# Performance work log

Hardware: AMD Instinct MI355X
Metric: run time of the kernel (lower is better)

Reference implementation:

```python
import jax, jax.numpy as jnp
import numpy as np

NUM_HEADS = 12
EPS = 1e-6


def setup_inputs() -> dict:
    key = jax.random.key(0)
    k1, k2, k3, k4, k5 = jax.random.split(key, 5)
    B, N, C = 8, 4096, 768
    scale = 1.0 / np.sqrt(C)
    return {
        "x": jax.random.normal(k1, (B, N, C), dtype=jnp.float32),
        "W_qkv": jax.random.normal(k2, (C, 3 * C), dtype=jnp.float32) * scale,
        "b_qkv": jax.random.normal(k3, (3 * C,), dtype=jnp.float32) * 0.02,
        "W_proj": jax.random.normal(k4, (C, C), dtype=jnp.float32) * scale,
        "b_proj": jax.random.normal(k5, (C,), dtype=jnp.float32) * 0.02,
    }


def reference(x, W_qkv, b_qkv, W_proj, b_proj):
    B, N, C = x.shape
    H = NUM_HEADS
    D = C // H
    # qkv projection -> (3, B, H, N, D)
    qkv = (x @ W_qkv + b_qkv).reshape(B, N, 3, H, D).transpose(2, 0, 3, 1, 4)
    q, k, v = qkv[0], qkv[1], qkv[2]
    q = jax.nn.sigmoid(q)
    k = jax.nn.sigmoid(k)
    ksum = k.sum(axis=2)  # [B,H,D]
    qsum = q.sum(axis=2)  # [B,H,D]
    # incoming/outgoing flow normalizers, [B,H,N]
    sink_incoming = 1.0 / (jnp.einsum('bhnd,bhd->bhn', q + EPS, ksum + EPS) + EPS)
    source_outgoing = 1.0 / (jnp.einsum('bhnd,bhd->bhn', k + EPS, qsum + EPS) + EPS)
    conserved_sink = jnp.einsum(
        'bhnd,bhd->bhn', q + EPS, (k * source_outgoing[..., None]).sum(axis=2) + EPS) + EPS
    conserved_source = jnp.einsum(
        'bhnd,bhd->bhn', k + EPS, (q * sink_incoming[..., None]).sum(axis=2) + EPS) + EPS
    conserved_source = jnp.clip(conserved_source, -1.0, 1.0)
    sink_allocation = jax.nn.sigmoid(conserved_sink * (float(N) / float(N)))
    source_competition = jax.nn.softmax(conserved_source, axis=-1) * float(N)
    # linear attention: kv = k^T @ (v * competition), [B,H,D,D]
    kv = jnp.einsum('bhnd,bhne->bhde', k, v * source_competition[..., None])
    x_update = jnp.einsum('bhnd,bhde->bhne', q, kv)
    x_update = x_update * sink_incoming[..., None] * sink_allocation[..., None]
    out = x_update.transpose(0, 2, 1, 3).reshape(B, N, C)
    out = out @ W_proj + b_proj
    return jax.nn.sigmoid(2.0 * out)
```

## Files before the change

### kernel.cpp

```cpp
#include <hip/hip_runtime.h>
#include <stdint.h>

#define EPSF 1e-6f

typedef unsigned short u16;
typedef __attribute__((ext_vector_type(8))) short short8;
typedef __attribute__((ext_vector_type(4))) float f32x4;

__device__ __forceinline__ float us2f(u16 u) {
  union { float f; unsigned int i; } c; c.i = ((unsigned int)u) << 16; return c.f;
}
__device__ __forceinline__ u16 f2bfu(float f) {
  union { float f; unsigned int i; } c; c.f = f;
  unsigned int i = c.i;
  return (u16)((i + 0x7FFFu + ((i >> 16) & 1u)) >> 16);
}
__device__ __forceinline__ float sigm(float x) { return 1.f / (1.f + __expf(-x)); }

typedef __attribute__((address_space(3))) unsigned int lds_u32;
typedef const __attribute__((address_space(1))) unsigned int glb_u32;
__device__ __forceinline__ void gl_lds16(const u16* g, u16* l) {
  __builtin_amdgcn_global_load_lds((glb_u32*)g, (lds_u32*)l, 16, 0, 0);
}

__global__ void k_cvt_x(const float* __restrict__ in, u16* __restrict__ out) {
  const int i = blockIdx.x * 256 + threadIdx.x;
  float4 v = ((const float4*)in)[i];
  ushort4 o;
  o.x = f2bfu(v.x); o.y = f2bfu(v.y); o.z = f2bfu(v.z); o.w = f2bfu(v.w);
  ((ushort4*)out)[i] = o;
}

__global__ void k_transpose(const float* __restrict__ in, u16* __restrict__ out, int R, int C) {
  __shared__ float tile[32][33];
  const int tx = threadIdx.x & 31, ty = threadIdx.x >> 5;
  const int c0 = blockIdx.x << 5, r0 = blockIdx.y << 5;
  for (int i = ty; i < 32; i += 8) tile[i][tx] = in[(size_t)(r0 + i) * C + c0 + tx];
  __syncthreads();
  for (int i = ty; i < 32; i += 8) out[(size_t)(c0 + i) * R + r0 + tx] = f2bfu(tile[tx][i]);
}

template <int MODE>
__global__ __launch_bounds__(512, 1) void k_gemm(
    const u16* __restrict__ A, const u16* __restrict__ BT,
    const float* __restrict__ bias,
    u16* __restrict__ qkvo, float* __restrict__ qsum, float* __restrict__ ksum,
    float* __restrict__ outf)
{
  __shared__ __align__(16) u16 smem[65536];
  const int tid = threadIdx.x;
  const int lane = tid & 63;
  const int wid = tid >> 6;
  const int wm = wid >> 2, wn = wid & 3;
  const int nx = gridDim.x;
  int lid = blockIdx.y * nx + blockIdx.x;
  const int q8 = (nx * gridDim.y) >> 3;
  lid = (lid & 7) * q8 + (lid >> 3);
  const int m0 = (lid / nx) << 8;
  const int n0 = (lid % nx) << 8;

  const int rowL0 = tid >> 3;
  const int gc = (tid & 7) ^ (rowL0 & 7);
  const u16* gA = A  + (size_t)(m0 + rowL0) * 768 + (gc << 3);
  const u16* gB = BT + (size_t)(n0 + rowL0) * 768 + (gc << 3);

  const int r16 = lane & 15;
  const int sgrp = lane >> 4;
  const int xk = r16 & 7;
  const int coff0 = ((sgrp) ^ xk) << 3;
  const int coff1 = ((4 + sgrp) ^ xk) << 3;
  const int bbase = ((wn & 1) << 6) + r16;

  f32x4 acc[8][4];
#pragma unroll
  for (int i = 0; i < 8; ++i)
#pragma unroll
    for (int j = 0; j < 4; ++j) acc[i][j] = (f32x4){0.f, 0.f, 0.f, 0.f};

#define STAGEU(tt, y)                                                         \
  do {                                                                        \
    u16* dst = &smem[(((((tt) & 1) << 2) | (y)) << 13) + (tid << 3)];         \
    const u16* s = (((y) < 2) ? gA + (size_t)(y) * 98304                      \
                              : gB + (size_t)((y) - 2) * 98304) + (tt) * 64;  \
    gl_lds16(s, dst);                                                         \
    gl_lds16(s + 49152, dst + 4096);                                          \
  } while (0)

#define RDA(mi, co) (*(const short8*)(pa + ((((mi) << 4) + r16) << 6) + (co)))
#define RDB(nj, co) (*(const short8*)(pb + ((bbase + ((nj) << 4)) << 6) + (co)))

#define MFMA16(P, A00, A01, A10, A11)                                                               \
  do {                                                                                              \
    acc[2*(P)  ][0] = __builtin_amdgcn_mfma_f32_16x16x32_bf16(A00, bf[0][0], acc[2*(P)  ][0],0,0,0);\
    acc[2*(P)  ][1] = __builtin_amdgcn_mfma_f32_16x16x32_bf16(A00, bf[1][0], acc[2*(P)  ][1],0,0,0);\
    acc[2*(P)  ][2] = __builtin_amdgcn_mfma_f32_16x16x32_bf16(A00, bf[2][0], acc[2*(P)  ][2],0,0,0);\
    acc[2*(P)  ][3] = __builtin_amdgcn_mfma_f32_16x16x32_bf16(A00, bf[3][0], acc[2*(P)  ][3],0,0,0);\
    acc[2*(P)+1][0] = __builtin_amdgcn_mfma_f32_16x16x32_bf16(A10, bf[0][0], acc[2*(P)+1][0],0,0,0);\
    acc[2*(P)+1][1] = __builtin_amdgcn_mfma_f32_16x16x32_bf16(A10, bf[1][0], acc[2*(P)+1][1],0,0,0);\
    acc[2*(P)+1][2] = __builtin_amdgcn_mfma_f32_16x16x32_bf16(A10, bf[2][0], acc[2*(P)+1][2],0,0,0);\
    acc[2*(P)+1][3] = __builtin_amdgcn_mfma_f32_16x16x32_bf16(A10, bf[3][0], acc[2*(P)+1][3],0,0,0);\
    acc[2*(P)  ][0] = __builtin_amdgcn_mfma_f32_16x16x32_bf16(A01, bf[0][1], acc[2*(P)  ][0],0,0,0);\
    acc[2*(P)  ][1] = __builtin_amdgcn_mfma_f32_16x16x32_bf16(A01, bf[1][1], acc[2*(P)  ][1],0,0,0);\
    acc[2*(P)  ][2] = __builtin_amdgcn_mfma_f32_16x16x32_bf16(A01, bf[2][1], acc[2*(P)  ][2],0,0,0);\
    acc[2*(P)  ][3] = __builtin_amdgcn_mfma_f32_16x16x32_bf16(A01, bf[3][1], acc[2*(P)  ][3],0,0,0);\
    acc[2*(P)+1][0] = __builtin_amdgcn_mfma_f32_16x16x32_bf16(A11, bf[0][1], acc[2*(P)+1][0],0,0,0);\
    acc[2*(P)+1][1] = __builtin_amdgcn_mfma_f32_16x16x32_bf16(A11, bf[1][1], acc[2*(P)+1][1],0,0,0);\
    acc[2*(P)+1][2] = __builtin_amdgcn_mfma_f32_16x16x32_bf16(A11, bf[2][1], acc[2*(P)+1][2],0,0,0);\
    acc[2*(P)+1][3] = __builtin_amdgcn_mfma_f32_16x16x32_bf16(A11, bf[3][1], acc[2*(P)+1][3],0,0,0);\
  } while (0)

#define PH_SYNC_PRE()                                          \
    __builtin_amdgcn_s_barrier();                              \
    asm volatile("s_waitcnt lgkmcnt(0)" ::: "memory");         \
    __builtin_amdgcn_sched_barrier(0);                         \
    __builtin_amdgcn_s_setprio(1)

#define PH_SYNC_POST()                                         \
    __builtin_amdgcn_s_setprio(0);                             \
    __builtin_amdgcn_sched_barrier(0);                         \
    __builtin_amdgcn_s_barrier()

  STAGEU(0, 0); STAGEU(0, 1); STAGEU(0, 2); STAGEU(0, 3);
  asm volatile("s_waitcnt vmcnt(0)" ::: "memory");
  __builtin_amdgcn_s_barrier();

  for (int t = 0; t < 12; ++t) {
    const u16* pa = &smem[((((t & 1) << 2) | wm) << 13)];
    const u16* pb = &smem[((((t & 1) << 2) | (2 + (wn >> 1))) << 13)];
    short8 bf[4][2];
    bf[0][0] = RDB(0, coff0); bf[0][1] = RDB(0, coff1);
    bf[1][0] = RDB(1, coff0); bf[1][1] = RDB(1, coff1);
    bf[2][0] = RDB(2, coff0); bf[2][1] = RDB(2, coff1);
    bf[3][0] = RDB(3, coff0); bf[3][1] = RDB(3, coff1);
    short8 a00 = RDA(0, coff0), a01 = RDA(0, coff1);
    short8 a10 = RDA(1, coff0), a11 = RDA(1, coff1);
    if (t < 11) { STAGEU(t + 1, 0); STAGEU(t + 1, 1); }
    PH_SYNC_PRE();
    MFMA16(0, a00, a01, a10, a11);
    PH_SYNC_POST();
    a00 = RDA(2, coff0); a01 = RDA(2, coff1);
    a10 = RDA(3, coff0); a11 = RDA(3, coff1);
    if (t < 11) { STAGEU(t + 1, 2); STAGEU(t + 1, 3); }
    PH_SYNC_PRE();
    MFMA16(1, a00, a01, a10, a11);
    PH_SYNC_POST();
    a00 = RDA(4, coff0); a01 = RDA(4, coff1);
    a10 = RDA(5, coff0); a11 = RDA(5, coff1);
    PH_SYNC_PRE();
    MFMA16(2, a00, a01, a10, a11);
    PH_SYNC_POST();
    a00 = RDA(6, coff0); a01 = RDA(6, coff1);
    a10 = RDA(7, coff0); a11 = RDA(7, coff1);
    PH_SYNC_PRE();
    MFMA16(3, a00, a01, a10, a11);
    __builtin_amdgcn_s_setprio(0);
    __builtin_amdgcn_sched_barrier(0);
    asm volatile("s_waitcnt vmcnt(0)" ::: "memory");
    __builtin_amdgcn_s_barrier();
  }
#undef PH_SYNC_PRE
#undef PH_SYNC_POST
#undef MFMA16
#undef RDA
#undef RDB
#undef STAGEU

  if (MODE == 0) {
    const int colc = n0 + (wn << 6);
    const bool sg = (colc < 1536);
    float jsum[4] = {0.f, 0.f, 0.f, 0.f};
#pragma unroll
    for (int mi = 0; mi < 8; ++mi) {
      const int rowb = m0 + (wm << 7) + (mi << 4) + ((lane >> 4) << 2);
#pragma unroll
      for (int nj = 0; nj < 4; ++nj) {
        const int col = colc + (nj << 4) + r16;
        const float bcol = bias[col];
        if (sg) {
#pragma unroll
          for (int rg = 0; rg < 4; ++rg) {
            const float val = sigm(acc[mi][nj][rg] + bcol);
            jsum[nj] += val;
            qkvo[(size_t)(rowb + rg) * 2304 + col] = f2bfu(val);
          }
        } else {
#pragma unroll
          for (int rg = 0; rg < 4; ++rg)
            qkvo[(size_t)(rowb + rg) * 2304 + col] = f2bfu(acc[mi][nj][rg] + bcol);
        }
      }
    }
    if (sg) {
#pragma unroll
      for (int nj = 0; nj < 4; ++nj) {
        jsum[nj] += __shfl_xor(jsum[nj], 16, 64);
        jsum[nj] += __shfl_xor(jsum[nj], 32, 64);
      }
      if (lane < 16) {
        const int b12 = (m0 >> 12) * 12;
        float* sdst = (colc >= 768) ? ksum : qsum;
        const int cb = (colc >= 768) ? colc - 768 : colc;
#pragma unroll
        for (int nj = 0; nj < 4; ++nj)
          atomicAdd(&sdst[(b12 << 6) + cb + (nj << 4) + r16], jsum[nj]);
      }
    }
  } else {
#pragma unroll
    for (int mi = 0; mi < 8; ++mi) {
      const int rowb = m0 + (wm << 7) + (mi << 4) + ((lane >> 4) << 2);
#pragma unroll
      for (int nj = 0; nj < 4; ++nj) {
        const int col = n0 + (wn << 6) + (nj << 4) + r16;
        const float bcol = bias[col];
#pragma unroll
        for (int rg = 0; rg < 4; ++rg)
          outf[(size_t)(rowb + rg) * 768 + col] = sigm(2.f * (acc[mi][nj][rg] + bcol));
      }
    }
  }
}

__global__ __launch_bounds__(256) void k_flow1(
    const u16* __restrict__ qkv,
    const float* __restrict__ qsum, const float* __restrict__ ksum,
    float* __restrict__ si_out, float* __restrict__ qsi, float* __restrict__ kso)
{
  const int bh = blockIdx.x >> 3, sp = blockIdx.x & 7;
  const int tid = threadIdx.x;
  const int grp = tid >> 3;
  const int d0 = (tid & 7) << 3;
  const u16* base = qkv + (size_t)(bh / 12) * 4096 * 2304 + (bh % 12) * 64;

  float ke[8], qe[8];
#pragma unroll
  for (int u = 0; u < 8; ++u) {
    ke[u] = ksum[(bh << 6) + d0 + u] + EPSF;
    qe[u] = qsum[(bh << 6) + d0 + u] + EPSF;
  }
  float Sk = 0.f, Sq = 0.f;
#pragma unroll
  for (int u = 0; u < 8; ++u) { Sk += ke[u]; Sq += qe[u]; }
#pragma unroll
  for (int m = 1; m < 8; m <<= 1) { Sk += __shfl_xor(Sk, m, 64); Sq += __shfl_xor(Sq, m, 64); }
  const float cK = EPSF * Sk + EPSF;
  const float cQ = EPSF * Sq + EPSF;

  float aq[8], ak[8];
#pragma unroll
  for (int u = 0; u < 8; ++u) { aq[u] = 0.f; ak[u] = 0.f; }

  const int nbase = sp << 9;
  for (int it = 0; it < 16; ++it) {
    const int n = nbase + (it << 5) + grp;
    const u16* rp = base + (size_t)n * 2304 + d0;
    short8 q8 = *(const short8*)(rp);
    short8 k8 = *(const short8*)(rp + 768);
    float dq = 0.f, dk = 0.f;
#pragma unroll
    for (int u = 0; u < 8; ++u) {
      dq += us2f((u16)q8[u]) * ke[u];
      dk += us2f((u16)k8[u]) * qe[u];
    }
#pragma unroll
    for (int m = 1; m < 8; m <<= 1) { dq += __shfl_xor(dq, m, 64); dk += __shfl_xor(dk, m, 64); }
    const float si = 1.f / (dq + cK);
    const float so = 1.f / (dk + cQ);
    if ((tid & 7) == 0) si_out[(bh << 12) + n] = si;
#pragma unroll
    for (int u = 0; u < 8; ++u) {
      aq[u] += us2f((u16)q8[u]) * si;
      ak[u] += us2f((u16)k8[u]) * so;
    }
  }
  __shared__ float redq[32][68];
  __shared__ float redk[32][68];
#pragma unroll
  for (int u = 0; u < 8; ++u) { redq[grp][d0 + u] = aq[u]; redk[grp][d0 + u] = ak[u]; }
  __syncthreads();
  if (tid < 128) {
    const int which = tid >> 6, d = tid & 63;
    float s = 0.f;
    if (which == 0) {
#pragma unroll
      for (int g = 0; g < 32; ++g) s += redq[g][d];
      atomicAdd(&qsi[(bh << 6) + d], s);
    } else {
#pragma unroll
      for (int g = 0; g < 32; ++g) s += redk[g][d];
      atomicAdd(&kso[(bh << 6) + d], s);
    }
  }
}

__global__ __launch_bounds__(256) void k_fkv(
    const u16* __restrict__ qkv,
    const float* __restrict__ qsi, const float* __restrict__ kso,
    const float* __restrict__ si_in,
    float* __restrict__ mo, float* __restrict__ sumexp, float* __restrict__ kvm)
{
  __shared__ __align__(16) u16 smem[2 * 64 * 136];
  u16* kT = smem;
  u16* vT = smem + 64 * 136;
  const int tid = threadIdx.x;
  const int bh = blockIdx.x >> 3, sp = blockIdx.x & 7;
  const int lane = tid & 63, wid = tid >> 6;
  const int r16 = lane & 15, g = lane >> 4;
  const u16* base = qkv + (size_t)(bh / 12) * 4096 * 2304 + (bh % 12) * 64;
  const float* sib = si_in + ((size_t)bh << 12);
  float* mob = mo + ((size_t)bh << 12);

  const int d0 = (tid & 7) << 3;
  float qie[8], soe[8];
#pragma unroll
  for (int u = 0; u < 8; ++u) {
    qie[u] = qsi[(bh << 6) + d0 + u] + EPSF;
    soe[u] = kso[(bh << 6) + d0 + u] + EPSF;
  }
  float Sq = qsi[(bh << 6) + lane] + EPSF;
  float Sk = kso[(bh << 6) + lane] + EPSF;
#pragma unroll
  for (int m = 1; m < 64; m <<= 1) { Sq += __shfl_xor(Sq, m, 64); Sk += __shfl_xor(Sk, m, 64); }
  const float cR = EPSF * Sq + EPSF;
  const float cS = EPSF * Sk + EPSF;

  f32x4 acc[4][4];
#pragma unroll
  for (int i = 0; i < 4; ++i)
#pragma unroll
    for (int j = 0; j < 4; ++j) acc[i][j] = (f32x4){0.f, 0.f, 0.f, 0.f};

  const int nf = (wid << 5) + (g << 3);
  float esum = 0.f;

  for (int st = 0; st < 4; ++st) {
    const int nst = (sp << 9) + (st << 7);
#pragma unroll
    for (int i = 0; i < 4; ++i) {
      const int c = tid + (i << 8);
      const int nl = c >> 3;
      const int ng = nst + nl;
      const u16* rp = base + (size_t)ng * 2304 + d0;
      short8 q8 = *(const short8*)(rp);
      short8 k8 = *(const short8*)(rp + 768);
      short8 v8 = *(const short8*)(rp + 1536);
      float pcs = 0.f, pcr = 0.f;
#pragma unroll
      for (int u = 0; u < 8; ++u) {
        pcs += us2f((u16)q8[u]) * soe[u];
        pcr += us2f((u16)k8[u]) * qie[u];
      }
#pragma unroll
      for (int m = 1; m < 8; m <<= 1) { pcs += __shfl_xor(pcs, m, 64); pcr += __shfl_xor(pcr, m, 64); }
      float cr = pcr + cR;
      cr = fminf(1.f, fmaxf(-1.f, cr));
      const float ev = __expf(cr);
      const int col = nl ^ (d0 & 56);
#pragma unroll
      for (int u = 0; u < 8; ++u) {
        kT[(d0 + u) * 136 + col] = f2bfu(us2f((u16)k8[u]) * ev);
        vT[(d0 + u) * 136 + col] = (u16)(unsigned short)v8[u];
      }
      if ((tid & 7) == 0) {
        mob[ng] = sib[ng] * sigm(pcs + cS);
        esum += ev;
      }
    }
    __syncthreads();

    short8 af[4], bf[4];
#pragma unroll
    for (int mi = 0; mi < 4; ++mi) {
      const int row = (mi << 4) + r16;
      af[mi] = *(const short8*)&kT[row * 136 + (nf ^ (row & 56))];
    }
#pragma unroll
    for (int nj = 0; nj < 4; ++nj) {
      const int row = (nj << 4) + r16;
      bf[nj] = *(const short8*)&vT[row * 136 + (nf ^ (row & 56))];
    }
#pragma unroll
    for (int mi = 0; mi < 4; ++mi)
#pragma unroll
      for (int nj = 0; nj < 4; ++nj)
        acc[mi][nj] = __builtin_amdgcn_mfma_f32_16x16x32_bf16(af[mi], bf[nj], acc[mi][nj], 0, 0, 0);
    __syncthreads();
  }

  float* red = (float*)smem;
  float* kvb = kvm + ((size_t)bh << 12);
#pragma unroll
  for (int half = 0; half < 2; ++half) {
#pragma unroll
    for (int m2 = 0; m2 < 2; ++m2) {
      const int mi = (half << 1) + m2;
#pragma unroll
      for (int nj = 0; nj < 4; ++nj)
#pragma unroll
        for (int rg = 0; rg < 4; ++rg)
          red[(wid << 11) + (((m2 << 4) + (g << 2) + rg) << 6) + (nj << 4) + r16] = acc[mi][nj][rg];
    }
    __syncthreads();
    const int base2 = tid << 3;
#pragma unroll
    for (int u2 = 0; u2 < 2; ++u2) {
      const int o = base2 + (u2 << 2);
      float4 s0 = *(const float4*)&red[o];
      float4 s1 = *(const float4*)&red[2048 + o];
      float4 s2 = *(const float4*)&red[4096 + o];
      float4 s3 = *(const float4*)&red[6144 + o];
      s0.x += s1.x + s2.x + s3.x;
      s0.y += s1.y + s2.y + s3.y;
      s0.z += s1.z + s2.z + s3.z;
      s0.w += s1.w + s2.w + s3.w;
      const int gi = (half << 11) + o;
      atomicAdd(&kvb[gi + 0], s0.x);
      atomicAdd(&kvb[gi + 1], s0.y);
      atomicAdd(&kvb[gi + 2], s0.z);
      atomicAdd(&kvb[gi + 3], s0.w);
    }
    __syncthreads();
  }

  esum += __shfl_xor(esum, 8, 64);
  esum += __shfl_xor(esum, 16, 64);
  esum += __shfl_xor(esum, 32, 64);
  if (lane == 0) atomicAdd(&sumexp[bh], esum);
}

__global__ __launch_bounds__(256) void k_xup(
    const u16* __restrict__ qkv, const float* __restrict__ kvm,
    const float* __restrict__ m_arr, const float* __restrict__ sumexp,
    u16* __restrict__ attn)
{
  const int bh = blockIdx.y;
  const int n0 = blockIdx.x << 7;
  const int b = bh / 12, h = bh % 12;
  __shared__ __align__(16) u16 qs[128 * 72];
  __shared__ __align__(16) u16 kvs[64 * 72];
  const int tid = threadIdx.x, lane = tid & 63, wid = tid >> 6;
  const u16* qg = qkv + (size_t)b * 4096 * 2304 + (size_t)n0 * 2304 + h * 64;
#pragma unroll
  for (int i = 0; i < 4; ++i) {
    const int c = tid + (i << 8);
    const int nl = c >> 3, d0 = (c & 7) << 3;
    *(short8*)&qs[nl * 72 + d0] = *(const short8*)(qg + (size_t)nl * 2304 + d0);
  }
  const float* kvg = kvm + ((size_t)bh << 12);
#pragma unroll
  for (int i = 0; i < 4; ++i) {
    const int idx = (tid << 2) + (i << 10);
    const int d = idx >> 6, e0 = idx & 63;
    float4 vv = *(const float4*)(kvg + idx);
    kvs[(e0 + 0) * 72 + d] = f2bfu(vv.x);
    kvs[(e0 + 1) * 72 + d] = f2bfu(vv.y);
    kvs[(e0 + 2) * 72 + d] = f2bfu(vv.z);
    kvs[(e0 + 3) * 72 + d] = f2bfu(vv.w);
  }
  __syncthreads();
  const float scale = 4096.f / sumexp[bh];
  const int r16 = lane & 15, kg8 = (lane >> 4) << 3;
  f32x4 acc[2][4];
#pragma unroll
  for (int i = 0; i < 2; ++i)
#pragma unroll
    for (int j = 0; j < 4; ++j) acc[i][j] = (f32x4){0.f, 0.f, 0.f, 0.f};
#pragma unroll
  for (int kk = 0; kk < 2; ++kk) {
    short8 af[2], bfv[4];
#pragma unroll
    for (int mi = 0; mi < 2; ++mi)
      af[mi] = *(const short8*)&qs[((wid << 5) + (mi << 4) + r16) * 72 + (kk << 5) + kg8];
#pragma unroll
    for (int nj = 0; nj < 4; ++nj)
      bfv[nj] = *(const short8*)&kvs[((nj << 4) + r16) * 72 + (kk << 5) + kg8];
#pragma unroll
    for (int mi = 0; mi < 2; ++mi)
#pragma unroll
      for (int nj = 0; nj < 4; ++nj)
        acc[mi][nj] = __builtin_amdgcn_mfma_f32_16x16x32_bf16(af[mi], bfv[nj], acc[mi][nj], 0, 0, 0);
  }
#pragma unroll
  for (int mi = 0; mi < 2; ++mi) {
#pragma unroll
    for (int rg = 0; rg < 4; ++rg) {
      const int n = n0 + (wid << 5) + (mi << 4) + ((lane >> 4) << 2) + rg;
      const float mult = m_arr[((size_t)bh << 12) + n] * scale;
#pragma unroll
      for (int nj = 0; nj < 4; ++nj) {
        const int e = (nj << 4) + r16;
        attn[((size_t)(b * 4096 + n)) * 768 + (h << 6) + e] = f2bfu(acc[mi][nj][rg] * mult);
      }
    }
  }
}

extern "C" void kernel_launch(void* const* d_in, const int* in_sizes, int n_in,
                              void* d_out, int out_size, void* d_ws, size_t ws_size,
                              hipStream_t stream)
{
  (void)in_sizes; (void)n_in; (void)out_size; (void)ws_size;
  const float* x     = (const float*)d_in[0];
  const float* Wqkv  = (const float*)d_in[1];
  const float* bqkv  = (const float*)d_in[2];
  const float* Wproj = (const float*)d_in[3];
  const float* bproj = (const float*)d_in[4];
  float* out = (float*)d_out;

  char* ws = (char*)d_ws;
  size_t off = 0;
  auto alloc = [&](size_t bytes) -> char* {
    char* p = ws + off;
    off += (bytes + 255) & ~(size_t)255;
    return p;
  };
  u16* qkv  = (u16*)alloc(150994944);
  u16* xbf  = (u16*)alloc(50331648);
  u16* WqT  = (u16*)alloc(3538944);
  u16* WpT  = (u16*)alloc(1179648);
  float* si = (float*)alloc(1572864);
  float* mb = (float*)alloc(1572864);
  char* zbase = ws + off;
  float* qsum   = (float*)alloc(24576);
  float* ksum   = (float*)alloc(24576);
  float* qsi    = (float*)alloc(24576);
  float* kso    = (float*)alloc(24576);
  float* sumexp = (float*)alloc(512);
  float* kvm    = (float*)alloc(1572864);
  const size_t zbytes = (size_t)((ws + off) - zbase);

  hipMemsetAsync(zbase, 0, zbytes, stream);
  k_cvt_x<<<24576, 256, 0, stream>>>(x, xbf);
  k_transpose<<<dim3(72, 24), 256, 0, stream>>>(Wqkv, WqT, 768, 2304);
  k_transpose<<<dim3(24, 24), 256, 0, stream>>>(Wproj, WpT, 768, 768);
  k_gemm<0><<<dim3(9, 128), 512, 0, stream>>>(xbf, WqT, bqkv, qkv, qsum, ksum, nullptr);
  k_flow1<<<768, 256, 0, stream>>>(qkv, qsum, ksum, si, qsi, kso);
  k_fkv<<<768, 256, 0, stream>>>(qkv, qsi, kso, si, mb, sumexp, kvm);
  k_xup<<<dim3(32, 96), 256, 0, stream>>>(qkv, kvm, mb, sumexp, xbf);
  k_gemm<1><<<dim3(3, 128), 512, 0, stream>>>(xbf, WpT, bproj, nullptr, nullptr, nullptr, out);
}
```

Before: 411.7 us.

## Merge prep kernels and move sink-allocation computation from k_fkv into k_xup

The x-to-bf16 conversion and the two weight transposes now run as one launch with block-index dispatch, which removes two kernel launches. The per-token sink allocation multiplier (sigmoid of q·(kso+eps)) was computed in k_fkv, which had to load q and write an mb array. It is now computed in k_xup from the q tile that kernel already loads, and kept in LDS. This drops the q loads and the mb global round-trip from k_fkv at the cost of a little extra arithmetic in k_xup.

```diff
diff --git a/kernel.cpp b/kernel.cpp
--- a/kernel.cpp
+++ b/kernel.cpp
@@ -23,18 +23,27 @@
   __builtin_amdgcn_global_load_lds((glb_u32*)g, (lds_u32*)l, 16, 0, 0);
 }
 
-__global__ void k_cvt_x(const float* __restrict__ in, u16* __restrict__ out) {
-  const int i = blockIdx.x * 256 + threadIdx.x;
-  float4 v = ((const float4*)in)[i];
-  ushort4 o;
-  o.x = f2bfu(v.x); o.y = f2bfu(v.y); o.z = f2bfu(v.z); o.w = f2bfu(v.w);
-  ((ushort4*)out)[i] = o;
-}
-
-__global__ void k_transpose(const float* __restrict__ in, u16* __restrict__ out, int R, int C) {
+__global__ void k_prep(const float* __restrict__ x, u16* __restrict__ xbf,
+                       const float* __restrict__ Wqkv, u16* __restrict__ WqT,
+                       const float* __restrict__ Wproj, u16* __restrict__ WpT) {
   __shared__ float tile[32][33];
+  const int b = blockIdx.x;
+  if (b < 24576) {
+    const int i = b * 256 + threadIdx.x;
+    float4 v = ((const float4*)x)[i];
+    ushort4 o;
+    o.x = f2bfu(v.x); o.y = f2bfu(v.y); o.z = f2bfu(v.z); o.w = f2bfu(v.w);
+    ((ushort4*)xbf)[i] = o;
+    return;
+  }
+  const float* in; u16* out; int R, C, bx, by;
+  if (b < 24576 + 1728) {
+    const int id = b - 24576; in = Wqkv; out = WqT; R = 768; C = 2304; bx = id % 72; by = id / 72;
+  } else {
+    const int id = b - 26304; in = Wproj; out = WpT; R = 768; C = 768; bx = id % 24; by = id / 24;
+  }
   const int tx = threadIdx.x & 31, ty = threadIdx.x >> 5;
-  const int c0 = blockIdx.x << 5, r0 = blockIdx.y << 5;
+  const int c0 = bx << 5, r0 = by << 5;
   for (int i = ty; i < 32; i += 8) tile[i][tx] = in[(size_t)(r0 + i) * C + c0 + tx];
   __syncthreads();
   for (int i = ty; i < 32; i += 8) out[(size_t)(c0 + i) * R + r0 + tx] = f2bfu(tile[tx][i]);
@@ -295,9 +304,8 @@
 
 __global__ __launch_bounds__(256) void k_fkv(
     const u16* __restrict__ qkv,
-    const float* __restrict__ qsi, const float* __restrict__ kso,
-    const float* __restrict__ si_in,
-    float* __restrict__ mo, float* __restrict__ sumexp, float* __restrict__ kvm)
+    const float* __restrict__ qsi,
+    float* __restrict__ sumexp, float* __restrict__ kvm)
 {
   __shared__ __align__(16) u16 smem[2 * 64 * 136];
   u16* kT = smem;
@@ -307,22 +315,15 @@
   const int lane = tid & 63, wid = tid >> 6;
   const int r16 = lane & 15, g = lane >> 4;
   const u16* base = qkv + (size_t)(bh / 12) * 4096 * 2304 + (bh % 12) * 64;
-  const float* sib = si_in + ((size_t)bh << 12);
-  float* mob = mo + ((size_t)bh << 12);
 
   const int d0 = (tid & 7) << 3;
-  float qie[8], soe[8];
-#pragma unroll
-  for (int u = 0; u < 8; ++u) {
-    qie[u] = qsi[(bh << 6) + d0 + u] + EPSF;
-    soe[u] = kso[(bh << 6) + d0 + u] + EPSF;
-  }
+  float qie[8];
+#pragma unroll
+  for (int u = 0; u < 8; ++u) qie[u] = qsi[(bh << 6) + d0 + u] + EPSF;
   float Sq = qsi[(bh << 6) + lane] + EPSF;
-  float Sk = kso[(bh << 6) + lane] + EPSF;
-#pragma unroll
-  for (int m = 1; m < 64; m <<= 1) { Sq += __shfl_xor(Sq, m, 64); Sk += __shfl_xor(Sk, m, 64); }
+#pragma unroll
+  for (int m = 1; m < 64; m <<= 1) Sq += __shfl_xor(Sq, m, 64);
   const float cR = EPSF * Sq + EPSF;
-  const float cS = EPSF * Sk + EPSF;
 
   f32x4 acc[4][4];
 #pragma unroll
@@ -341,17 +342,13 @@
       const int nl = c >> 3;
       const int ng = nst + nl;
       const u16* rp = base + (size_t)ng * 2304 + d0;
-      short8 q8 = *(const short8*)(rp);
       short8 k8 = *(const short8*)(rp + 768);
       short8 v8 = *(const short8*)(rp + 1536);
-      float pcs = 0.f, pcr = 0.f;
-#pragma unroll
-      for (int u = 0; u < 8; ++u) {
-        pcs += us2f((u16)q8[u]) * soe[u];
-        pcr += us2f((u16)k8[u]) * qie[u];
-      }
-#pragma unroll
-      for (int m = 1; m < 8; m <<= 1) { pcs += __shfl_xor(pcs, m, 64); pcr += __shfl_xor(pcr, m, 64); }
+      float pcr = 0.f;
+#pragma unroll
+      for (int u = 0; u < 8; ++u) pcr += us2f((u16)k8[u]) * qie[u];
+#pragma unroll
+      for (int m = 1; m < 8; m <<= 1) pcr += __shfl_xor(pcr, m, 64);
       float cr = pcr + cR;
       cr = fminf(1.f, fmaxf(-1.f, cr));
       const float ev = __expf(cr);
@@ -361,10 +358,7 @@
         kT[(d0 + u) * 136 + col] = f2bfu(us2f((u16)k8[u]) * ev);
         vT[(d0 + u) * 136 + col] = (u16)(unsigned short)v8[u];
       }
-      if ((tid & 7) == 0) {
-        mob[ng] = sib[ng] * sigm(pcs + cS);
-        esum += ev;
-      }
+      if ((tid & 7) == 0) esum += ev;
     }
     __syncthreads();
 
@@ -430,7 +424,8 @@
 
 __global__ __launch_bounds__(256) void k_xup(
     const u16* __restrict__ qkv, const float* __restrict__ kvm,
-    const float* __restrict__ m_arr, const float* __restrict__ sumexp,
+    const float* __restrict__ si_arr, const float* __restrict__ kso,
+    const float* __restrict__ sumexp,
     u16* __restrict__ attn)
 {
   const int bh = blockIdx.y;
@@ -438,13 +433,34 @@
   const int b = bh / 12, h = bh % 12;
   __shared__ __align__(16) u16 qs[128 * 72];
   __shared__ __align__(16) u16 kvs[64 * 72];
+  __shared__ float m_lds[128];
   const int tid = threadIdx.x, lane = tid & 63, wid = tid >> 6;
+  const int d0c = (tid & 7) << 3;
+
+  float soe[8];
+#pragma unroll
+  for (int u = 0; u < 8; ++u) soe[u] = kso[(bh << 6) + d0c + u] + EPSF;
+  float Ss = 0.f;
+#pragma unroll
+  for (int u = 0; u < 8; ++u) Ss += soe[u];
+#pragma unroll
+  for (int m = 1; m < 8; m <<= 1) Ss += __shfl_xor(Ss, m, 64);
+  const float cS = EPSF * Ss + EPSF;
+
   const u16* qg = qkv + (size_t)b * 4096 * 2304 + (size_t)n0 * 2304 + h * 64;
 #pragma unroll
   for (int i = 0; i < 4; ++i) {
     const int c = tid + (i << 8);
     const int nl = c >> 3, d0 = (c & 7) << 3;
-    *(short8*)&qs[nl * 72 + d0] = *(const short8*)(qg + (size_t)nl * 2304 + d0);
+    short8 q8 = *(const short8*)(qg + (size_t)nl * 2304 + d0);
+    *(short8*)&qs[nl * 72 + d0] = q8;
+    float pcs = 0.f;
+#pragma unroll
+    for (int u = 0; u < 8; ++u) pcs += us2f((u16)q8[u]) * soe[u];
+#pragma unroll
+    for (int m = 1; m < 8; m <<= 1) pcs += __shfl_xor(pcs, m, 64);
+    if ((tid & 7) == 0)
+      m_lds[nl] = si_arr[((size_t)bh << 12) + n0 + nl] * sigm(pcs + cS);
   }
   const float* kvg = kvm + ((size_t)bh << 12);
 #pragma unroll
@@ -484,8 +500,9 @@
   for (int mi = 0; mi < 2; ++mi) {
 #pragma unroll
     for (int rg = 0; rg < 4; ++rg) {
-      const int n = n0 + (wid << 5) + (mi << 4) + ((lane >> 4) << 2) + rg;
-      const float mult = m_arr[((size_t)bh << 12) + n] * scale;
+      const int nloc = (wid << 5) + (mi << 4) + ((lane >> 4) << 2) + rg;
+      const int n = n0 + nloc;
+      const float mult = m_lds[nloc] * scale;
 #pragma unroll
       for (int nj = 0; nj < 4; ++nj) {
         const int e = (nj << 4) + r16;
@@ -519,7 +536,6 @@
   u16* WqT  = (u16*)alloc(3538944);
   u16* WpT  = (u16*)alloc(1179648);
   float* si = (float*)alloc(1572864);
-  float* mb = (float*)alloc(1572864);
   char* zbase = ws + off;
   float* qsum   = (float*)alloc(24576);
   float* ksum   = (float*)alloc(24576);
@@ -530,12 +546,10 @@
   const size_t zbytes = (size_t)((ws + off) - zbase);
 
   hipMemsetAsync(zbase, 0, zbytes, stream);
-  k_cvt_x<<<24576, 256, 0, stream>>>(x, xbf);
-  k_transpose<<<dim3(72, 24), 256, 0, stream>>>(Wqkv, WqT, 768, 2304);
-  k_transpose<<<dim3(24, 24), 256, 0, stream>>>(Wproj, WpT, 768, 768);
+  k_prep<<<26880, 256, 0, stream>>>(x, xbf, Wqkv, WqT, Wproj, WpT);
   k_gemm<0><<<dim3(9, 128), 512, 0, stream>>>(xbf, WqT, bqkv, qkv, qsum, ksum, nullptr);
   k_flow1<<<768, 256, 0, stream>>>(qkv, qsum, ksum, si, qsi, kso);
-  k_fkv<<<768, 256, 0, stream>>>(qkv, qsi, kso, si, mb, sumexp, kvm);
-  k_xup<<<dim3(32, 96), 256, 0, stream>>>(qkv, kvm, mb, sumexp, xbf);
+  k_fkv<<<768, 256, 0, stream>>>(qkv, qsi, sumexp, kvm);
+  k_xup<<<dim3(32, 96), 256, 0, stream>>>(qkv, kvm, si, kso, sumexp, xbf);
   k_gemm<1><<<dim3(3, 128), 512, 0, stream>>>(xbf, WpT, bproj, nullptr, nullptr, nullptr, out);
 }
```

Measured after the change: 391.8 us. 1.05x faster.
